# Performance work log

Hardware: AMD Instinct MI355X
Metric: run time of the kernel (lower is better)

The kernel has to match this reference:

```python
import jax, jax.numpy as jnp
import numpy as np

B, S, H = 32, 2048, 1024

def setup_inputs() -> dict:
    key = jax.random.key(0)
    k1, k2, k3, k4 = jax.random.split(key, 4)
    scale_w = 1.0 / np.sqrt(3 * H)
    scale_v = 1.0 / np.sqrt(H)
    return {
        "enc_output": jax.random.normal(k1, (B, S, 2 * H), dtype=jnp.float32),
        "enc_mask": jnp.ones((B, S, 1), dtype=jnp.float32),
        "dec_hidden": jax.random.normal(k2, (1, B, H), dtype=jnp.float32),
        "W_w": jax.random.normal(k3, (H, 3 * H), dtype=jnp.float32) * scale_w,
        "W_b": jnp.zeros((H,), dtype=jnp.float32),
        "V_w": jax.random.normal(k4, (1, H), dtype=jnp.float32) * scale_v,
        "V_b": jnp.zeros((1,), dtype=jnp.float32),
    }


def reference(enc_output, enc_mask, dec_hidden, W_w, W_b, V_w, V_b):
    # enc_output: (B, S, 2H); enc_mask: (B, S, 1); dec_hidden: (1, B, H)
    b, s, _ = enc_output.shape
    h = dec_hidden.shape[-1]
    dec = jnp.broadcast_to(jnp.transpose(dec_hidden, (1, 0, 2)), (b, s, h))  # (B,S,H)
    x = jnp.concatenate([enc_output, dec], axis=-1)                          # (B,S,3H)
    energy = jnp.tanh(jnp.einsum('bsk,hk->bsh', x, W_w) + W_b)               # (B,S,H)
    scores = jnp.einsum('bsh,oh->bso', energy, V_w)[..., 0] + V_b[0]         # (B,S)
    keep = enc_mask[..., 0] > 0  # original masks where (1 - mask) is True
    scores = jnp.where(keep, scores, -jnp.inf)
    attn = jax.nn.softmax(scores, axis=-1)                                   # (B,S)
    context = jnp.einsum('bs,bsd->bd', attn, enc_output)                     # (B,2H)
    return context
```

## Files before the change

kernel.cpp:

```cpp
#include <hip/hip_runtime.h>
#include <hip/hip_bf16.h>
#include <math.h>

#define B_   32
#define S_   2048
#define H_   1024
#define K2H  2048
#define M_TOT (B_*S_)

typedef __attribute__((ext_vector_type(8))) short bf16x8;
typedef __attribute__((ext_vector_type(4))) float f32x4;

__device__ __forceinline__ short f2bf(float f) {
    union { float f; unsigned u; } c; c.f = f;
    unsigned u = c.u;
    unsigned r = u + 0x7FFFu + ((u >> 16) & 1u);
    return (short)(r >> 16);
}

__device__ __forceinline__ float ftanh(float x) {
    x = fminf(fmaxf(x, -15.f), 15.f);
    float e = __expf(2.f * x);
    return (e - 1.f) / (e + 1.f);
}

__device__ __forceinline__ void bar() {
    asm volatile("" ::: "memory");
    __builtin_amdgcn_s_barrier();
    asm volatile("" ::: "memory");
}

__device__ __forceinline__ void gload16(const short* g, short* l) {
    __builtin_amdgcn_global_load_lds(
        (const __attribute__((address_space(1))) void*)g,
        (__attribute__((address_space(3))) void*)l,
        16, 0, 0);
}

__global__ void prep_kernel(const float* __restrict__ enc, short* __restrict__ encb,
                            const float* __restrict__ Ww, short* __restrict__ w1,
                            const float* __restrict__ dec, const float* __restrict__ Wb,
                            float* __restrict__ dproj) {
    int bid = blockIdx.x;
    int t = threadIdx.x;
    if (bid < 65536) {
        size_t e = ((size_t)bid * 256 + t) * 8;
        float4 v0 = *reinterpret_cast<const float4*>(enc + e);
        float4 v1 = *reinterpret_cast<const float4*>(enc + e + 4);
        short s[8];
        s[0]=f2bf(v0.x); s[1]=f2bf(v0.y); s[2]=f2bf(v0.z); s[3]=f2bf(v0.w);
        s[4]=f2bf(v1.x); s[5]=f2bf(v1.y); s[6]=f2bf(v1.z); s[7]=f2bf(v1.w);
        *reinterpret_cast<int4*>(encb + e) = *reinterpret_cast<const int4*>(s);
    } else if (bid < 65536 + 2048) {
        int idx = (bid - 65536) * 256 + t;
        int e = idx * 4;
        int h = e >> 11;
        int k = e & 2047;
        float4 v = *reinterpret_cast<const float4*>(Ww + (size_t)h * 3072 + k);
        short4 o;
        o.x = f2bf(v.x); o.y = f2bf(v.y); o.z = f2bf(v.z); o.w = f2bf(v.w);
        *reinterpret_cast<short4*>(w1 + (size_t)h * 2048 + k) = o;
    } else {
        __shared__ float dl[1024];
        int db = bid - 65536 - 2048;
        int b = db >> 4;
        int hc = db & 15;
        for (int i = t; i < 1024; i += 256) dl[i] = dec[b * 1024 + i];
        __syncthreads();
        int wv = t >> 6, lane = t & 63;
        for (int it = 0; it < 16; ++it) {
            int h = hc * 64 + wv * 16 + it;
            const float* wrow = Ww + (size_t)h * 3072 + 2048;
            float acc = 0.f;
            for (int j = lane; j < 1024; j += 64) acc += dl[j] * wrow[j];
            for (int m = 32; m >= 1; m >>= 1) acc += __shfl_xor(acc, m);
            if (lane == 0) dproj[b * 1024 + h] = acc + Wb[h];
        }
    }
}

#define NT_ 64

#define STAGE(dst, src, T) do { \
    _Pragma("unroll") \
    for (int u = 0; u < 2; ++u) { \
        int lr = u * 128 + sr; \
        int cs = (sc ^ ((lr >> 1) & 3)) * 8; \
        gload16((src) + (size_t)lr * K2H + (T) * 32 + cs, (dst) + lr * 32 + sc * 8); \
    } } while (0)

#define RDA(dstf, AS, roff) do { \
    _Pragma("unroll") \
    for (int ii = 0; ii < 4; ++ii) { \
        int R = wm * 128 + (roff) + ii * 16 + (lane & 15); \
        dstf[ii] = *reinterpret_cast<const bf16x8*>(&(AS)[R * 32 + (((lane >> 4) ^ ((R >> 1) & 3)) * 8)]); \
    } } while (0)

#define RDB(dstf, BS) do { \
    _Pragma("unroll") \
    for (int jj = 0; jj < 4; ++jj) { \
        int R = wn * 64 + jj * 16 + (lane & 15); \
        dstf[jj] = *reinterpret_cast<const bf16x8*>(&(BS)[R * 32 + (((lane >> 4) ^ ((R >> 1) & 3)) * 8)]); \
    } } while (0)

#define TILE(T, AS, BS, APF, BPF) do { \
    RDA(aF, AS, 0); \
    RDB(bF, BS); \
    RDA(aG, AS, 64); \
    if ((T) + 3 < NT_) { STAGE(APF, abase, (T) + 3); STAGE(BPF, bbase, (T) + 3); } \
    __builtin_amdgcn_s_setprio(1); \
    _Pragma("unroll") for (int ii = 0; ii < 4; ++ii) \
      _Pragma("unroll") for (int jj = 0; jj < 4; ++jj) \
        acc[ii][jj] = __builtin_amdgcn_mfma_f32_16x16x32_bf16(aF[ii], bF[jj], acc[ii][jj], 0, 0, 0); \
    _Pragma("unroll") for (int ii = 0; ii < 4; ++ii) \
      _Pragma("unroll") for (int jj = 0; jj < 4; ++jj) \
        acc[4+ii][jj] = __builtin_amdgcn_mfma_f32_16x16x32_bf16(aG[ii], bF[jj], acc[4+ii][jj], 0, 0, 0); \
    __builtin_amdgcn_s_setprio(0); \
    __builtin_amdgcn_sched_group_barrier(0x100, 12, 0);  \
    __builtin_amdgcn_sched_group_barrier(0x008,  8, 0); \
    __builtin_amdgcn_sched_group_barrier(0x020,  1, 0);  \
    __builtin_amdgcn_sched_group_barrier(0x008,  8, 0); \
    __builtin_amdgcn_sched_group_barrier(0x020,  1, 0); \
    __builtin_amdgcn_sched_group_barrier(0x008,  8, 0); \
    __builtin_amdgcn_sched_group_barrier(0x020,  1, 0); \
    __builtin_amdgcn_sched_group_barrier(0x008,  8, 0); \
    __builtin_amdgcn_sched_group_barrier(0x020,  1, 0); \
    if ((T) <= NT_ - 4)      { asm volatile("s_waitcnt vmcnt(8)" ::: "memory"); } \
    else if ((T) == NT_ - 3) { asm volatile("s_waitcnt vmcnt(4)" ::: "memory"); } \
    else if ((T) == NT_ - 2) { asm volatile("s_waitcnt vmcnt(0)" ::: "memory"); } \
    bar(); \
} while (0)

__launch_bounds__(512, 1)
__global__ void fused_gemm8(const short* __restrict__ encb, const short* __restrict__ w1,
                            const float* __restrict__ dproj, const float* __restrict__ Vw,
                            float* __restrict__ scores_p) {
    __shared__ short A0[8192], A1[8192], A2[8192], A3[8192];
    __shared__ short B0[8192], B1[8192], B2[8192], B3[8192];
    int bid = blockIdx.x;
    int x = bid & 7, r = bid >> 3;
    int nt = r & 3;
    int mt = ((r >> 2) << 3) | x;
    int m0 = mt * 256, n0 = nt * 256;
    int t5 = threadIdx.x, lane = t5 & 63, wv = t5 >> 6;
    int wm = wv >> 2, wn = wv & 3;

    int sr = t5 >> 2;
    int sc = t5 & 3;
    const short* abase = encb + (size_t)m0 * K2H;
    const short* bbase = w1 + (size_t)n0 * K2H;

    f32x4 acc[8][4] = {};
    bf16x8 aF[4], aG[4], bF[4];

    STAGE(A0, abase, 0); STAGE(B0, bbase, 0);
    STAGE(A1, abase, 1); STAGE(B1, bbase, 1);
    STAGE(A2, abase, 2); STAGE(B2, bbase, 2);
    asm volatile("s_waitcnt vmcnt(8)" ::: "memory");
    bar();

    for (int to = 0; to < NT_ / 4; ++to) {
        int T = to * 4;
        TILE(T,     A0, B0, A3, B3);
        TILE(T + 1, A1, B1, A0, B0);
        TILE(T + 2, A2, B2, A1, B1);
        TILE(T + 3, A3, B3, A2, B2);
    }

    int b = m0 >> 11;
    float dp[4], vvv[4];
#pragma unroll
    for (int j = 0; j < 4; ++j) {
        int hg = n0 + wn * 64 + j * 16 + (lane & 15);
        dp[j] = dproj[b * 1024 + hg];
        vvv[j] = Vw[hg];
    }
    float* sp = scores_p + (size_t)(nt * 4 + wn) * M_TOT;
#pragma unroll
    for (int i = 0; i < 8; ++i) {
#pragma unroll
        for (int q = 0; q < 4; ++q) {
            float part = 0.f;
#pragma unroll
            for (int j = 0; j < 4; ++j)
                part += vvv[j] * ftanh(acc[i][j][q] + dp[j]);
            part += __shfl_xor(part, 1);
            part += __shfl_xor(part, 2);
            part += __shfl_xor(part, 4);
            part += __shfl_xor(part, 8);
            if ((lane & 15) == 0) {
                int mg = m0 + wm * 128 + i * 16 + ((lane >> 4) << 2) + q;
                sp[mg] = part;
            }
        }
    }
}

__global__ void sumscores_kernel(const float* __restrict__ scores_p, float* __restrict__ scores) {
    int m = blockIdx.x * 256 + threadIdx.x;
    float s = 0.f;
#pragma unroll
    for (int p = 0; p < 16; ++p) s += scores_p[(size_t)p * M_TOT + m];
    scores[m] = s;
}

__global__ void softmax_kernel(const float* __restrict__ scores, const float* __restrict__ mask,
                               float* __restrict__ attn) {
    int b = blockIdx.x;
    int t = threadIdx.x;
    __shared__ float red[8];
    __shared__ float red2[8];
    float v[8];
    float mx = -INFINITY;
#pragma unroll
    for (int k = 0; k < 8; ++k) {
        int s = t + k * 256;
        float xv = scores[b * 2048 + s];
        float mk = mask[b * 2048 + s];
        xv = (mk > 0.f) ? xv : -INFINITY;
        v[k] = xv;
        mx = fmaxf(mx, xv);
    }
    int lane = t & 63, wv = t >> 6;
    for (int m = 32; m >= 1; m >>= 1) mx = fmaxf(mx, __shfl_xor(mx, m));
    if (lane == 0) red[wv] = mx;
    __syncthreads();
    mx = fmaxf(fmaxf(red[0], red[1]), fmaxf(red[2], red[3]));
    float sum = 0.f;
#pragma unroll
    for (int k = 0; k < 8; ++k) { v[k] = __expf(v[k] - mx); sum += v[k]; }
    for (int m = 32; m >= 1; m >>= 1) sum += __shfl_xor(sum, m);
    if (lane == 0) red2[wv] = sum;
    __syncthreads();
    sum = red2[0] + red2[1] + red2[2] + red2[3];
    float inv = 1.f / sum;
#pragma unroll
    for (int k = 0; k < 8; ++k) attn[b * 2048 + t + k * 256] = v[k] * inv;
}

__global__ void context_kernel(const short* __restrict__ encb, const float* __restrict__ attn,
                               float* __restrict__ out) {
    __shared__ float aw[2048];
    __shared__ float red[8][256];
    int bid = blockIdx.x;
    int b = bid >> 3;
    int dc = bid & 7;
    int t = threadIdx.x;
#pragma unroll
    for (int k = 0; k < 8; ++k) aw[t + k * 256] = attn[b * 2048 + t + k * 256];
    __syncthreads();
    int rgrp = t >> 5;
    int cg = t & 31;
    const short* base = encb + (size_t)b * S_ * K2H + dc * 256 + cg * 8;
    float acc[8] = {};
#pragma unroll 4
    for (int i = 0; i < 256; ++i) {
        int s = i * 8 + rgrp;
        float w = aw[s];
        bf16x8 v = *reinterpret_cast<const bf16x8*>(base + (size_t)s * K2H);
#pragma unroll
        for (int j = 0; j < 8; ++j) {
            union { unsigned u; float f; } cv;
            cv.u = ((unsigned)(unsigned short)v[j]) << 16;
            acc[j] += w * cv.f;
        }
    }
#pragma unroll
    for (int j = 0; j < 8; ++j) red[rgrp][cg * 8 + j] = acc[j];
    __syncthreads();
    float s = 0.f;
#pragma unroll
    for (int r2 = 0; r2 < 8; ++r2) s += red[r2][t];
    out[b * 2048 + dc * 256 + t] = s;
}

extern "C" void kernel_launch(void* const* d_in, const int* in_sizes, int n_in,
                              void* d_out, int out_size, void* d_ws, size_t ws_size,
                              hipStream_t stream) {
    const float* enc  = (const float*)d_in[0];
    const float* mask = (const float*)d_in[1];
    const float* dec  = (const float*)d_in[2];
    const float* Ww   = (const float*)d_in[3];
    const float* Wb   = (const float*)d_in[4];
    const float* Vw   = (const float*)d_in[5];
    float* out = (float*)d_out;

    char* ws = (char*)d_ws;
    const size_t ENC_B = (size_t)M_TOT * K2H * 2;
    short* encb     = (short*)ws;
    short* w1       = (short*)(ws + ENC_B);
    float* scores_p = (float*)(ws + ENC_B + (4u << 20));
    float* dproj    = (float*)(ws + ENC_B + (8u << 20));
    float* attn     = (float*)(ws + ENC_B + (8u << 20) + (128u << 10));
    float* scores   = (float*)(ws + ENC_B + (8u << 20) + (384u << 10));

    prep_kernel<<<68096, 256, 0, stream>>>(enc, encb, Ww, w1, dec, Wb, dproj);
    fused_gemm8<<<1024, 512, 0, stream>>>(encb, w1, dproj, Vw, scores_p);
    sumscores_kernel<<<256, 256, 0, stream>>>(scores_p, scores);
    softmax_kernel<<<32, 256, 0, stream>>>(scores, mask, attn);
    context_kernel<<<256, 256, 0, stream>>>(encb, attn, out);
}
```

Measured before the change: 577.8 us.

## Fuse encoder fp32-to-bf16 conversion into GEMM LDS reads and drop the bf16 copy

The separate pass that converted the whole encoder output to bf16 is removed. The GEMM now streams fp32 tiles of the encoder output into LDS and packs them to bf16 with v_cvt_pk_bf16_f32 when loading MFMA fragments, and the context kernel reads fp32 directly. This is meant to eliminate a full read-plus-write pass over the largest tensor. In exchange, the GEMM's A tiles double in size, which cuts the LDS pipeline from four stages to three, and the context kernel now reads twice as many bytes.

```diff
diff --git a/kernel.cpp b/kernel.cpp
--- a/kernel.cpp
+++ b/kernel.cpp
@@ -37,22 +37,20 @@
         16, 0, 0);
 }
 
-__global__ void prep_kernel(const float* __restrict__ enc, short* __restrict__ encb,
-                            const float* __restrict__ Ww, short* __restrict__ w1,
-                            const float* __restrict__ dec, const float* __restrict__ Wb,
-                            float* __restrict__ dproj) {
+__device__ __forceinline__ void gload16f(const float* g, float* l) {
+    __builtin_amdgcn_global_load_lds(
+        (const __attribute__((address_space(1))) void*)g,
+        (__attribute__((address_space(3))) void*)l,
+        16, 0, 0);
+}
+
+__global__ void prep_small(const float* __restrict__ Ww, short* __restrict__ w1,
+                           const float* __restrict__ dec, const float* __restrict__ Wb,
+                           float* __restrict__ dproj) {
     int bid = blockIdx.x;
     int t = threadIdx.x;
-    if (bid < 65536) {
-        size_t e = ((size_t)bid * 256 + t) * 8;
-        float4 v0 = *reinterpret_cast<const float4*>(enc + e);
-        float4 v1 = *reinterpret_cast<const float4*>(enc + e + 4);
-        short s[8];
-        s[0]=f2bf(v0.x); s[1]=f2bf(v0.y); s[2]=f2bf(v0.z); s[3]=f2bf(v0.w);
-        s[4]=f2bf(v1.x); s[5]=f2bf(v1.y); s[6]=f2bf(v1.z); s[7]=f2bf(v1.w);
-        *reinterpret_cast<int4*>(encb + e) = *reinterpret_cast<const int4*>(s);
-    } else if (bid < 65536 + 2048) {
-        int idx = (bid - 65536) * 256 + t;
+    if (bid < 2048) {
+        int idx = bid * 256 + t;
         int e = idx * 4;
         int h = e >> 11;
         int k = e & 2047;
@@ -62,7 +60,7 @@
         *reinterpret_cast<short4*>(w1 + (size_t)h * 2048 + k) = o;
     } else {
         __shared__ float dl[1024];
-        int db = bid - 65536 - 2048;
+        int db = bid - 2048;
         int b = db >> 4;
         int hc = db & 15;
         for (int i = t; i < 1024; i += 256) dl[i] = dec[b * 1024 + i];
@@ -81,19 +79,36 @@
 
 #define NT_ 64
 
-#define STAGE(dst, src, T) do { \
+#define STAGEA(dst, T) do { \
+    _Pragma("unroll") \
+    for (int u = 0; u < 4; ++u) { \
+        int lr = u * 64 + sra; \
+        int cs = (sca ^ (lr & 7)) * 4; \
+        gload16f(abase + (size_t)lr * K2H + (T) * 32 + cs, (dst) + lr * 32 + sca * 4); \
+    } } while (0)
+
+#define STAGEB(dst, T) do { \
     _Pragma("unroll") \
     for (int u = 0; u < 2; ++u) { \
-        int lr = u * 128 + sr; \
-        int cs = (sc ^ ((lr >> 1) & 3)) * 8; \
-        gload16((src) + (size_t)lr * K2H + (T) * 32 + cs, (dst) + lr * 32 + sc * 8); \
+        int lr = u * 128 + srb; \
+        int cs = (scb ^ ((lr >> 1) & 3)) * 8; \
+        gload16(bbase + (size_t)lr * K2H + (T) * 32 + cs, (dst) + lr * 32 + scb * 8); \
     } } while (0)
 
-#define RDA(dstf, AS, roff) do { \
+#define RDAF(dstf, AS, roff) do { \
     _Pragma("unroll") \
     for (int ii = 0; ii < 4; ++ii) { \
         int R = wm * 128 + (roff) + ii * 16 + (lane & 15); \
-        dstf[ii] = *reinterpret_cast<const bf16x8*>(&(AS)[R * 32 + (((lane >> 4) ^ ((R >> 1) & 3)) * 8)]); \
+        int rs_ = R & 7; \
+        int kq_ = lane >> 4; \
+        float4 lo_ = *reinterpret_cast<const float4*>(&(AS)[R * 32 + (((2*kq_)   ^ rs_) * 4)]); \
+        float4 hi_ = *reinterpret_cast<const float4*>(&(AS)[R * 32 + (((2*kq_+1) ^ rs_) * 4)]); \
+        union { unsigned u[4]; bf16x8 v8; } pk_; \
+        asm("v_cvt_pk_bf16_f32 %0, %1, %2" : "=v"(pk_.u[0]) : "v"(lo_.x), "v"(lo_.y)); \
+        asm("v_cvt_pk_bf16_f32 %0, %1, %2" : "=v"(pk_.u[1]) : "v"(lo_.z), "v"(lo_.w)); \
+        asm("v_cvt_pk_bf16_f32 %0, %1, %2" : "=v"(pk_.u[2]) : "v"(hi_.x), "v"(hi_.y)); \
+        asm("v_cvt_pk_bf16_f32 %0, %1, %2" : "=v"(pk_.u[3]) : "v"(hi_.z), "v"(hi_.w)); \
+        dstf[ii] = pk_.v8; \
     } } while (0)
 
 #define RDB(dstf, BS) do { \
@@ -104,10 +119,10 @@
     } } while (0)
 
 #define TILE(T, AS, BS, APF, BPF) do { \
-    RDA(aF, AS, 0); \
+    RDAF(aF, AS, 0); \
     RDB(bF, BS); \
-    RDA(aG, AS, 64); \
-    if ((T) + 3 < NT_) { STAGE(APF, abase, (T) + 3); STAGE(BPF, bbase, (T) + 3); } \
+    RDAF(aG, AS, 64); \
+    if ((T) + 2 < NT_) { STAGEA(APF, (T) + 2); STAGEB(BPF, (T) + 2); } \
     __builtin_amdgcn_s_setprio(1); \
     _Pragma("unroll") for (int ii = 0; ii < 4; ++ii) \
       _Pragma("unroll") for (int jj = 0; jj < 4; ++jj) \
@@ -116,27 +131,30 @@
       _Pragma("unroll") for (int jj = 0; jj < 4; ++jj) \
         acc[4+ii][jj] = __builtin_amdgcn_mfma_f32_16x16x32_bf16(aG[ii], bF[jj], acc[4+ii][jj], 0, 0, 0); \
     __builtin_amdgcn_s_setprio(0); \
-    __builtin_amdgcn_sched_group_barrier(0x100, 12, 0);  \
-    __builtin_amdgcn_sched_group_barrier(0x008,  8, 0); \
-    __builtin_amdgcn_sched_group_barrier(0x020,  1, 0);  \
-    __builtin_amdgcn_sched_group_barrier(0x008,  8, 0); \
-    __builtin_amdgcn_sched_group_barrier(0x020,  1, 0); \
-    __builtin_amdgcn_sched_group_barrier(0x008,  8, 0); \
-    __builtin_amdgcn_sched_group_barrier(0x020,  1, 0); \
-    __builtin_amdgcn_sched_group_barrier(0x008,  8, 0); \
-    __builtin_amdgcn_sched_group_barrier(0x020,  1, 0); \
-    if ((T) <= NT_ - 4)      { asm volatile("s_waitcnt vmcnt(8)" ::: "memory"); } \
-    else if ((T) == NT_ - 3) { asm volatile("s_waitcnt vmcnt(4)" ::: "memory"); } \
+    __builtin_amdgcn_sched_group_barrier(0x008, 5, 0); \
+    __builtin_amdgcn_sched_group_barrier(0x020, 1, 0); \
+    __builtin_amdgcn_sched_group_barrier(0x008, 5, 0); \
+    __builtin_amdgcn_sched_group_barrier(0x020, 1, 0); \
+    __builtin_amdgcn_sched_group_barrier(0x008, 5, 0); \
+    __builtin_amdgcn_sched_group_barrier(0x020, 1, 0); \
+    __builtin_amdgcn_sched_group_barrier(0x008, 5, 0); \
+    __builtin_amdgcn_sched_group_barrier(0x020, 1, 0); \
+    __builtin_amdgcn_sched_group_barrier(0x008, 5, 0); \
+    __builtin_amdgcn_sched_group_barrier(0x020, 1, 0); \
+    __builtin_amdgcn_sched_group_barrier(0x008, 5, 0); \
+    __builtin_amdgcn_sched_group_barrier(0x020, 1, 0); \
+    __builtin_amdgcn_sched_group_barrier(0x008, 2, 0); \
+    if ((T) <= NT_ - 3)      { asm volatile("s_waitcnt vmcnt(6)" ::: "memory"); } \
     else if ((T) == NT_ - 2) { asm volatile("s_waitcnt vmcnt(0)" ::: "memory"); } \
     bar(); \
 } while (0)
 
 __launch_bounds__(512, 1)
-__global__ void fused_gemm8(const short* __restrict__ encb, const short* __restrict__ w1,
+__global__ void fused_gemm8(const float* __restrict__ enc, const short* __restrict__ w1,
                             const float* __restrict__ dproj, const float* __restrict__ Vw,
                             float* __restrict__ scores_p) {
-    __shared__ short A0[8192], A1[8192], A2[8192], A3[8192];
-    __shared__ short B0[8192], B1[8192], B2[8192], B3[8192];
+    __shared__ float A0[8192], A1[8192], A2[8192];
+    __shared__ short B0[8192], B1[8192], B2[8192];
     int bid = blockIdx.x;
     int x = bid & 7, r = bid >> 3;
     int nt = r & 3;
@@ -145,27 +163,26 @@
     int t5 = threadIdx.x, lane = t5 & 63, wv = t5 >> 6;
     int wm = wv >> 2, wn = wv & 3;
 
-    int sr = t5 >> 2;
-    int sc = t5 & 3;
-    const short* abase = encb + (size_t)m0 * K2H;
+    int sra = t5 >> 3, sca = t5 & 7;
+    int srb = t5 >> 2, scb = t5 & 3;
+    const float* abase = enc + (size_t)m0 * K2H;
     const short* bbase = w1 + (size_t)n0 * K2H;
 
     f32x4 acc[8][4] = {};
     bf16x8 aF[4], aG[4], bF[4];
 
-    STAGE(A0, abase, 0); STAGE(B0, bbase, 0);
-    STAGE(A1, abase, 1); STAGE(B1, bbase, 1);
-    STAGE(A2, abase, 2); STAGE(B2, bbase, 2);
-    asm volatile("s_waitcnt vmcnt(8)" ::: "memory");
+    STAGEA(A0, 0); STAGEB(B0, 0);
+    STAGEA(A1, 1); STAGEB(B1, 1);
+    asm volatile("s_waitcnt vmcnt(6)" ::: "memory");
     bar();
 
-    for (int to = 0; to < NT_ / 4; ++to) {
-        int T = to * 4;
-        TILE(T,     A0, B0, A3, B3);
+    for (int to = 0; to < 21; ++to) {
+        int T = to * 3;
+        TILE(T,     A0, B0, A2, B2);
         TILE(T + 1, A1, B1, A0, B0);
         TILE(T + 2, A2, B2, A1, B1);
-        TILE(T + 3, A3, B3, A2, B2);
-    }
+    }
+    TILE(63, A0, B0, A1, B1);
 
     int b = m0 >> 11;
     float dp[4], vvv[4];
@@ -238,7 +255,7 @@
     for (int k = 0; k < 8; ++k) attn[b * 2048 + t + k * 256] = v[k] * inv;
 }
 
-__global__ void context_kernel(const short* __restrict__ encb, const float* __restrict__ attn,
+__global__ void context_kernel(const float* __restrict__ enc, const float* __restrict__ attn,
                                float* __restrict__ out) {
     __shared__ float aw[2048];
     __shared__ float red[8][256];
@@ -251,19 +268,16 @@
     __syncthreads();
     int rgrp = t >> 5;
     int cg = t & 31;
-    const short* base = encb + (size_t)b * S_ * K2H + dc * 256 + cg * 8;
+    const float* base = enc + (size_t)b * S_ * K2H + dc * 256 + cg * 8;
     float acc[8] = {};
 #pragma unroll 4
     for (int i = 0; i < 256; ++i) {
         int s = i * 8 + rgrp;
         float w = aw[s];
-        bf16x8 v = *reinterpret_cast<const bf16x8*>(base + (size_t)s * K2H);
-#pragma unroll
-        for (int j = 0; j < 8; ++j) {
-            union { unsigned u; float f; } cv;
-            cv.u = ((unsigned)(unsigned short)v[j]) << 16;
-            acc[j] += w * cv.f;
-        }
+        float4 v0 = *reinterpret_cast<const float4*>(base + (size_t)s * K2H);
+        float4 v1 = *reinterpret_cast<const float4*>(base + (size_t)s * K2H + 4);
+        acc[0] += w * v0.x; acc[1] += w * v0.y; acc[2] += w * v0.z; acc[3] += w * v0.w;
+        acc[4] += w * v1.x; acc[5] += w * v1.y; acc[6] += w * v1.z; acc[7] += w * v1.w;
     }
 #pragma unroll
     for (int j = 0; j < 8; ++j) red[rgrp][cg * 8 + j] = acc[j];
@@ -286,17 +300,15 @@
     float* out = (float*)d_out;
 
     char* ws = (char*)d_ws;
-    const size_t ENC_B = (size_t)M_TOT * K2H * 2;
-    short* encb     = (short*)ws;
-    short* w1       = (short*)(ws + ENC_B);
-    float* scores_p = (float*)(ws + ENC_B + (4u << 20));
-    float* dproj    = (float*)(ws + ENC_B + (8u << 20));
-    float* attn     = (float*)(ws + ENC_B + (8u << 20) + (128u << 10));
-    float* scores   = (float*)(ws + ENC_B + (8u << 20) + (384u << 10));
-
-    prep_kernel<<<68096, 256, 0, stream>>>(enc, encb, Ww, w1, dec, Wb, dproj);
-    fused_gemm8<<<1024, 512, 0, stream>>>(encb, w1, dproj, Vw, scores_p);
+    short* w1       = (short*)ws;
+    float* scores_p = (float*)(ws + (4u << 20));
+    float* dproj    = (float*)(ws + (8u << 20));
+    float* attn     = (float*)(ws + (8u << 20) + (128u << 10));
+    float* scores   = (float*)(ws + (8u << 20) + (384u << 10));
+
+    prep_small<<<2560, 256, 0, stream>>>(Ww, w1, dec, Wb, dproj);
+    fused_gemm8<<<1024, 512, 0, stream>>>(enc, w1, dproj, Vw, scores_p);
     sumscores_kernel<<<256, 256, 0, stream>>>(scores_p, scores);
     softmax_kernel<<<32, 256, 0, stream>>>(scores, mask, attn);
-    context_kernel<<<256, 256, 0, stream>>>(encb, attn, out);
-}
+    context_kernel<<<256, 256, 0, stream>>>(enc, attn, out);
+}
```

Result: slower. 624.9 us (+8.1%).
